# Performance work log

Measured on AMD Instinct MI355X. Metric: run time of the kernel, lower is better.

Reference implementation:

```python
import jax, jax.numpy as jnp
import numpy as np

C = 512

def conv1x1(x, w, b):
    # x: [B,C,H,W], w: [O,C], b: [O]
    return jnp.einsum('bchw,oc->bohw', x, w) + b[None, :, None, None]

def setup_inputs() -> dict:
    key = jax.random.key(0)
    ks = jax.random.split(key, 7)
    s = 1.0 / np.sqrt(C)
    x = jax.random.normal(ks[0], (8, C, 64, 64), dtype=jnp.float32)
    wq = jax.random.uniform(ks[1], (C, C), jnp.float32, -s, s)
    bq = jax.random.uniform(ks[2], (C,), jnp.float32, -s, s)
    wk = jax.random.uniform(ks[3], (C, C), jnp.float32, -s, s)
    bk = jax.random.uniform(ks[4], (C,), jnp.float32, -s, s)
    wv = jax.random.uniform(ks[5], (C, C), jnp.float32, -s, s)
    bv = jax.random.uniform(ks[6], (C,), jnp.float32, -s, s)
    return {"x": x, "wq": wq, "bq": bq, "wk": wk, "bk": bk, "wv": wv, "bv": bv}

def reference(x, wq, bq, wk, bk, wv, bv):
    B, Cc, H, W = x.shape
    q = conv1x1(x, wq, bq).reshape(B, Cc, H * W)   # [B,C,N]
    k = conv1x1(x, wk, bk).reshape(B, Cc, H * W)   # [B,C,N]
    v = conv1x1(x, wv, bv).reshape(B, Cc, H * W)   # [B,C,N]
    attn = jnp.einsum('bcn,bdn->bcd', q, k)        # q @ k^T over spatial dim -> [B,C,C]
    attn = jax.nn.softmax(attn, axis=-1)
    out = jnp.einsum('bcd,bdn->bcn', attn, v).reshape(B, Cc, H, W)
    return out + x
```

## Files before the change

kernel.cpp:

```cpp
#include <hip/hip_runtime.h>
#include <cstdint>

typedef unsigned short u16;
typedef unsigned int   u32;
typedef _Float16 f16;

typedef __attribute__((ext_vector_type(8))) _Float16 f16x8;
typedef __attribute__((ext_vector_type(4))) float    f32x4;

__device__ __forceinline__ u16 f2h(float f) {
    union { f16 h; u16 u; } c; c.h = (f16)f; return c.u;
}
__device__ __forceinline__ float h2f(u16 u) {
    union { u16 u; f16 h; } c; c.u = u; return (float)c.h;
}

__device__ __forceinline__ void async_copy16(const u16* g, u16* lds) {
    __builtin_amdgcn_global_load_lds(
        (const __attribute__((address_space(1))) void*)g,
        (__attribute__((address_space(3))) void*)lds,
        16, 0, 0);
}

__device__ __forceinline__ void gemm_nt_f16(
    u16* smem, const u16* __restrict__ A, int lda,
    const u16* __restrict__ B, int ldb, int K, f32x4 acc[4][4])
{
    u16* As = smem; u16* Bs = smem + 4096;
    const int t = threadIdx.x, w = t >> 6, lane = t & 63;
    const int srow = lane >> 2;
    const int skc  = (((lane & 3) ^ ((lane >> 3) & 3)) * 8);
    const int ra0 = (w*2+0)*16 + srow, ra1 = (w*2+1)*16 + srow;
    const u16* gA0 = A + (size_t)ra0 * lda + skc;
    const u16* gA1 = A + (size_t)ra1 * lda + skc;
    const u16* gB0 = B + (size_t)ra0 * ldb + skc;
    const u16* gB1 = B + (size_t)ra1 * ldb + skc;
    u16* lA0 = As + (w*2+0)*512; u16* lA1 = As + (w*2+1)*512;
    u16* lB0 = Bs + (w*2+0)*512; u16* lB1 = Bs + (w*2+1)*512;
    const int fr = lane & 15, fq = lane >> 4;
    const int fc = (fq ^ ((fr >> 1) & 3)) * 8;
    const int wm = (w >> 1) * 64, wn = (w & 1) * 64;
    const u16* fA = As + (wm + fr) * 32 + fc;
    const u16* fB = Bs + (wn + fr) * 32 + fc;

    for (int k0 = 0; k0 < K; k0 += 32) {
        async_copy16(gA0 + k0, lA0);
        async_copy16(gA1 + k0, lA1);
        async_copy16(gB0 + k0, lB0);
        async_copy16(gB1 + k0, lB1);
        __syncthreads();
        f16x8 af[4], bf[4];
#pragma unroll
        for (int i = 0; i < 4; i++) af[i] = *(const f16x8*)(fA + i * 512);
#pragma unroll
        for (int i = 0; i < 4; i++) bf[i] = *(const f16x8*)(fB + i * 512);
#pragma unroll
        for (int mi = 0; mi < 4; mi++)
#pragma unroll
            for (int ni = 0; ni < 4; ni++)
                acc[mi][ni] = __builtin_amdgcn_mfma_f32_16x16x32_f16(
                    af[mi], bf[ni], acc[mi][ni], 0, 0, 0);
        __syncthreads();
    }
}

__device__ __forceinline__ void zero_acc(f32x4 acc[4][4]) {
#pragma unroll
    for (int i = 0; i < 4; i++)
#pragma unroll
        for (int j = 0; j < 4; j++) {
            f32x4 z = {0.f, 0.f, 0.f, 0.f};
            acc[i][j] = z;
        }
}

__global__ __launch_bounds__(256) void k_convw(const float* __restrict__ wq,
                                               const float* __restrict__ wk,
                                               const float* __restrict__ wv,
                                               u16* __restrict__ Wf)
{
    const int t = blockIdx.x * 256 + threadIdx.x;
    const int e = t * 4;
    const int sel = e >> 18;
    const int off = e & 262143;
    const float* src = (sel == 0) ? wq : (sel == 1) ? wk : wv;
    float4 v = *(const float4*)(src + off);
    ushort4 h;
    h.x = f2h(v.x); h.y = f2h(v.y); h.z = f2h(v.z); h.w = f2h(v.w);
    *(ushort4*)(Wf + sel * 262144 + off) = h;
}

__global__ __launch_bounds__(256) void k_transpose(const float* __restrict__ x,
                                                   u16* __restrict__ XT)
{
    __shared__ u16 tile[64][70];
    const int t  = threadIdx.x;
    const int b  = blockIdx.z;
    const int c0 = blockIdx.y * 64;
    const int n0 = blockIdx.x * 64;
    const int rr   = t >> 4;
    const int col4 = (t & 15) * 4;

    const float* src = x + ((size_t)b * 512 + c0) * 4096 + n0;
#pragma unroll
    for (int i = 0; i < 4; i++) {
        int row = i * 16 + rr;
        float4 v = *(const float4*)(src + (size_t)row * 4096 + col4);
        ushort4 h;
        h.x = f2h(v.x); h.y = f2h(v.y); h.z = f2h(v.z); h.w = f2h(v.w);
        *(ushort4*)&tile[row][col4] = h;
    }
    __syncthreads();
    u16* dst = XT + ((size_t)b * 4096 + n0) * 512 + c0;
#pragma unroll
    for (int i = 0; i < 4; i++) {
        int nrow = i * 16 + rr;
        ushort4 o;
        o.x = tile[col4 + 0][nrow];
        o.y = tile[col4 + 1][nrow];
        o.z = tile[col4 + 2][nrow];
        o.w = tile[col4 + 3][nrow];
        *(ushort4*)(dst + (size_t)nrow * 512 + col4) = o;
    }
}

__global__ __launch_bounds__(256) void k_qkv(
    const u16* __restrict__ Wf,
    const float* __restrict__ bq, const float* __restrict__ bk, const float* __restrict__ bv,
    const u16* __restrict__ XT,
    u16* __restrict__ Qh, u16* __restrict__ Kh, u16* __restrict__ VT)
{
    __shared__ u16 smem[8192];
    const int n0  = blockIdx.x * 128;
    const int my  = blockIdx.y;
    const int b   = blockIdx.z;
    const int sel = my >> 2;
    const int m0  = (my & 3) * 128;

    const float* bi = (sel == 0) ? bq : (sel == 1) ? bk : bv;
    const u16* Ap = Wf + (size_t)sel * 262144 + (size_t)m0 * 512;
    const u16* Bp = XT + ((size_t)b * 4096 + n0) * 512;

    f32x4 acc[4][4];
    zero_acc(acc);
    gemm_nt_f16(smem, Ap, 512, Bp, 512, 512, acc);

    const int t = threadIdx.x, w = t >> 6, lane = t & 63;
    const int wm = (w >> 1) * 64, wn = (w & 1) * 64;
    const int cn = lane & 15, cq = lane >> 4;

    if (sel < 2) {
        u16* out = ((sel == 0) ? Qh : Kh) + (size_t)b * 512 * 4096;
#pragma unroll
        for (int mi = 0; mi < 4; mi++)
#pragma unroll
            for (int ni = 0; ni < 4; ni++)
#pragma unroll
                for (int r = 0; r < 4; r++) {
                    int m = wm + mi * 16 + cq * 4 + r;
                    int n = wn + ni * 16 + cn;
                    out[(size_t)(m0 + m) * 4096 + n0 + n] =
                        f2h(acc[mi][ni][r] + bi[m0 + m]);
                }
    } else {
        u16* out = VT + (size_t)b * 4096 * 512;
#pragma unroll
        for (int mi = 0; mi < 4; mi++)
#pragma unroll
            for (int ni = 0; ni < 4; ni++) {
                int n  = wn + ni * 16 + cn;
                int mb = wm + mi * 16 + cq * 4;
                ushort4 pk;
                pk.x = f2h(acc[mi][ni][0] + bi[m0 + mb + 0]);
                pk.y = f2h(acc[mi][ni][1] + bi[m0 + mb + 1]);
                pk.z = f2h(acc[mi][ni][2] + bi[m0 + mb + 2]);
                pk.w = f2h(acc[mi][ni][3] + bi[m0 + mb + 3]);
                *(ushort4*)(out + (size_t)(n0 + n) * 512 + m0 + mb) = pk;
            }
    }
}

__global__ __launch_bounds__(256) void k_scores(const u16* __restrict__ Qh,
                                                const u16* __restrict__ Kh,
                                                float* __restrict__ S)
{
    __shared__ u16 smem[8192];
    const int n0 = blockIdx.x * 128;
    const int m0 = blockIdx.y * 128;
    const int bz = blockIdx.z;
    const int b  = bz >> 2, ks = bz & 3;

    const u16* Ap = Qh + (size_t)b * 512 * 4096 + (size_t)m0 * 4096 + ks * 1024;
    const u16* Bp = Kh + (size_t)b * 512 * 4096 + (size_t)n0 * 4096 + ks * 1024;

    f32x4 acc[4][4];
    zero_acc(acc);
    gemm_nt_f16(smem, Ap, 4096, Bp, 4096, 1024, acc);

    const int t = threadIdx.x, w = t >> 6, lane = t & 63;
    const int wm = (w >> 1) * 64, wn = (w & 1) * 64;
    const int cn = lane & 15, cq = lane >> 4;

    float* out = S + ((size_t)(ks * 8 + b) * 512 + m0) * 512 + n0;
#pragma unroll
    for (int mi = 0; mi < 4; mi++)
#pragma unroll
        for (int ni = 0; ni < 4; ni++)
#pragma unroll
            for (int r = 0; r < 4; r++) {
                int m = wm + mi * 16 + cq * 4 + r;
                int n = wn + ni * 16 + cn;
                out[(size_t)m * 512 + n] = acc[mi][ni][r];
            }
}

__global__ __launch_bounds__(256) void k_softmax(const float* __restrict__ S,
                                                 u16* __restrict__ P)
{
    const int row = blockIdx.x;
    const int t = threadIdx.x, w = t >> 6, lane = t & 63;
    const size_t st = (size_t)8 * 512 * 512;
    const float* r0 = S + (size_t)row * 512;

    float v0 = r0[t]       + r0[t + st]       + r0[t + 2*st]       + r0[t + 3*st];
    float v1 = r0[t + 256] + r0[t + 256 + st] + r0[t + 256 + 2*st] + r0[t + 256 + 3*st];

    float m = fmaxf(v0, v1);
    for (int o = 32; o; o >>= 1) m = fmaxf(m, __shfl_xor(m, o));
    __shared__ float redm[4];
    if (lane == 0) redm[w] = m;
    __syncthreads();
    m = fmaxf(fmaxf(redm[0], redm[1]), fmaxf(redm[2], redm[3]));

    float e0 = __expf(v0 - m), e1 = __expf(v1 - m);
    float s = e0 + e1;
    for (int o = 32; o; o >>= 1) s += __shfl_xor(s, o);
    __shared__ float reds[4];
    if (lane == 0) reds[w] = s;
    __syncthreads();
    s = reds[0] + reds[1] + reds[2] + reds[3];

    float inv = 1.0f / s;
    P[(size_t)row * 512 + t]       = f2h(e0 * inv);
    P[(size_t)row * 512 + t + 256] = f2h(e1 * inv);
}

__global__ __launch_bounds__(256) void k_out(const u16* __restrict__ P,
                                             const u16* __restrict__ VT,
                                             const float* __restrict__ x,
                                             float* __restrict__ out)
{
    __shared__ u16 smem[8192];
    const int n0 = blockIdx.x * 128;
    const int m0 = blockIdx.y * 128;
    const int b  = blockIdx.z;

    const u16* Ap = P  + (size_t)b * 512 * 512 + (size_t)m0 * 512;
    const u16* Bp = VT + (size_t)b * 4096 * 512 + (size_t)n0 * 512;

    f32x4 acc[4][4];
    zero_acc(acc);
    gemm_nt_f16(smem, Ap, 512, Bp, 512, 512, acc);

    const int t = threadIdx.x, w = t >> 6, lane = t & 63;
    const int wm = (w >> 1) * 64, wn = (w & 1) * 64;
    const int cn = lane & 15, cq = lane >> 4;

#pragma unroll
    for (int mi = 0; mi < 4; mi++)
#pragma unroll
        for (int ni = 0; ni < 4; ni++)
#pragma unroll
            for (int r = 0; r < 4; r++) {
                int m = wm + mi * 16 + cq * 4 + r;
                int n = wn + ni * 16 + cn;
                size_t idx = ((size_t)b * 512 + m0 + m) * 4096 + n0 + n;
                out[idx] = acc[mi][ni][r] + x[idx];
            }
}

extern "C" void kernel_launch(void* const* d_in, const int* in_sizes, int n_in,
                              void* d_out, int out_size, void* d_ws, size_t ws_size,
                              hipStream_t stream)
{
    const float* x  = (const float*)d_in[0];
    const float* wq = (const float*)d_in[1];
    const float* bq = (const float*)d_in[2];
    const float* wk = (const float*)d_in[3];
    const float* bk = (const float*)d_in[4];
    const float* wv = (const float*)d_in[5];
    const float* bv = (const float*)d_in[6];
    float* out = (float*)d_out;

    char* ws = (char*)d_ws;
    u16*  Wf = (u16*)(ws);
    u16*  XT = (u16*)(ws + 1572864);
    u16*  Qh = (u16*)(ws + 35127296);
    u16*  Kh = (u16*)(ws + 68681728);
    u16*  VT = (u16*)(ws + 102236160);
    float* S = (float*)(ws + 1572864);
    u16*  P  = (u16*)(ws + 135790592);

    k_convw<<<dim3(768), dim3(256), 0, stream>>>(wq, wk, wv, Wf);
    k_transpose<<<dim3(64, 8, 8), dim3(256), 0, stream>>>(x, XT);
    k_qkv<<<dim3(32, 12, 8), dim3(256), 0, stream>>>(Wf, bq, bk, bv, XT, Qh, Kh, VT);
    k_scores<<<dim3(4, 4, 32), dim3(256), 0, stream>>>(Qh, Kh, S);
    k_softmax<<<dim3(4096), dim3(256), 0, stream>>>(S, P);
    k_out<<<dim3(32, 4, 8), dim3(256), 0, stream>>>(P, VT, x, out);
}
```

Before: 295.2 us.

## Fuse x transpose and fp16 conversion into QKV GEMM B-tile loading

Removes the separate transpose kernel and the XT workspace. The QKV GEMM now reads fp32 x directly, converts it to fp16 in registers and writes it transposed into a swizzled LDS tile. The next k-slice is prefetched into registers while the current MFMAs run. This avoids writing and re-reading a 32MB intermediate and one launch. The cost is that x is re-read as fp32 by 12 blocks per tile (across m and q/k/v) with strided scalar loads instead of async LDS copies.

```diff
diff --git a/kernel.cpp b/kernel.cpp
--- a/kernel.cpp
+++ b/kernel.cpp
@@ -10,9 +10,6 @@
 
 __device__ __forceinline__ u16 f2h(float f) {
     union { f16 h; u16 u; } c; c.h = (f16)f; return c.u;
-}
-__device__ __forceinline__ float h2f(u16 u) {
-    union { u16 u; f16 h; } c; c.u = u; return (float)c.h;
 }
 
 __device__ __forceinline__ void async_copy16(const u16* g, u16* lds) {
@@ -90,47 +87,14 @@
     *(ushort4*)(Wf + sel * 262144 + off) = h;
 }
 
-__global__ __launch_bounds__(256) void k_transpose(const float* __restrict__ x,
-                                                   u16* __restrict__ XT)
-{
-    __shared__ u16 tile[64][70];
-    const int t  = threadIdx.x;
-    const int b  = blockIdx.z;
-    const int c0 = blockIdx.y * 64;
-    const int n0 = blockIdx.x * 64;
-    const int rr   = t >> 4;
-    const int col4 = (t & 15) * 4;
-
-    const float* src = x + ((size_t)b * 512 + c0) * 4096 + n0;
-#pragma unroll
-    for (int i = 0; i < 4; i++) {
-        int row = i * 16 + rr;
-        float4 v = *(const float4*)(src + (size_t)row * 4096 + col4);
-        ushort4 h;
-        h.x = f2h(v.x); h.y = f2h(v.y); h.z = f2h(v.z); h.w = f2h(v.w);
-        *(ushort4*)&tile[row][col4] = h;
-    }
-    __syncthreads();
-    u16* dst = XT + ((size_t)b * 4096 + n0) * 512 + c0;
-#pragma unroll
-    for (int i = 0; i < 4; i++) {
-        int nrow = i * 16 + rr;
-        ushort4 o;
-        o.x = tile[col4 + 0][nrow];
-        o.y = tile[col4 + 1][nrow];
-        o.z = tile[col4 + 2][nrow];
-        o.w = tile[col4 + 3][nrow];
-        *(ushort4*)(dst + (size_t)nrow * 512 + col4) = o;
-    }
-}
-
 __global__ __launch_bounds__(256) void k_qkv(
     const u16* __restrict__ Wf,
     const float* __restrict__ bq, const float* __restrict__ bk, const float* __restrict__ bv,
-    const u16* __restrict__ XT,
+    const float* __restrict__ x,
     u16* __restrict__ Qh, u16* __restrict__ Kh, u16* __restrict__ VT)
 {
     __shared__ u16 smem[8192];
+    u16* As = smem; u16* Bs = smem + 4096;
     const int n0  = blockIdx.x * 128;
     const int my  = blockIdx.y;
     const int b   = blockIdx.z;
@@ -138,15 +102,71 @@
     const int m0  = (my & 3) * 128;
 
     const float* bi = (sel == 0) ? bq : (sel == 1) ? bk : bv;
-    const u16* Ap = Wf + (size_t)sel * 262144 + (size_t)m0 * 512;
-    const u16* Bp = XT + ((size_t)b * 4096 + n0) * 512;
+    const u16* A = Wf + (size_t)sel * 262144 + (size_t)m0 * 512;
+
+    const int t = threadIdx.x, w = t >> 6, lane = t & 63;
+
+    const int srow = lane >> 2;
+    const int skc  = (((lane & 3) ^ ((lane >> 3) & 3)) * 8);
+    const int ra0 = (w*2+0)*16 + srow, ra1 = (w*2+1)*16 + srow;
+    const u16* gA0 = A + (size_t)ra0 * 512 + skc;
+    const u16* gA1 = A + (size_t)ra1 * 512 + skc;
+    u16* lA0 = As + (w*2+0)*512; u16* lA1 = As + (w*2+1)*512;
+
+    const int nn = t & 15;
+    const int cg = t >> 4;
+    const float* xb = x + ((size_t)b * 512 + 2 * cg) * 4096 + n0 + nn;
+    const int chunkB = (cg >> 2) ^ ((nn >> 1) & 3);
+    u16* lB = Bs + nn * 32 + chunkB * 8 + ((2 * cg) & 7);
+
+    const int fr = lane & 15, fq = lane >> 4;
+    const int fc = (fq ^ ((fr >> 1) & 3)) * 8;
+    const int wm = (w >> 1) * 64, wn = (w & 1) * 64;
+    const u16* fA = As + (wm + fr) * 32 + fc;
+    const u16* fB = Bs + (wn + fr) * 32 + fc;
 
     f32x4 acc[4][4];
     zero_acc(acc);
-    gemm_nt_f16(smem, Ap, 512, Bp, 512, 512, acc);
-
-    const int t = threadIdx.x, w = t >> 6, lane = t & 63;
-    const int wm = (w >> 1) * 64, wn = (w & 1) * 64;
+
+    float va[8], vb[8];
+#pragma unroll
+    for (int nb = 0; nb < 8; nb++) {
+        va[nb] = xb[nb * 16];
+        vb[nb] = xb[4096 + nb * 16];
+    }
+
+    for (int k0 = 0; k0 < 512; k0 += 32) {
+        async_copy16(gA0 + k0, lA0);
+        async_copy16(gA1 + k0, lA1);
+#pragma unroll
+        for (int nb = 0; nb < 8; nb++) {
+            u32 pk = (u32)f2h(va[nb]) | ((u32)f2h(vb[nb]) << 16);
+            *(u32*)(lB + nb * 512) = pk;
+        }
+        __syncthreads();
+
+        const int kn = (k0 + 32 < 512) ? (k0 + 32) : 0;
+        const float* xk = xb + (size_t)kn * 4096;
+#pragma unroll
+        for (int nb = 0; nb < 8; nb++) {
+            va[nb] = xk[nb * 16];
+            vb[nb] = xk[4096 + nb * 16];
+        }
+
+        f16x8 af[4], bf[4];
+#pragma unroll
+        for (int i = 0; i < 4; i++) af[i] = *(const f16x8*)(fA + i * 512);
+#pragma unroll
+        for (int i = 0; i < 4; i++) bf[i] = *(const f16x8*)(fB + i * 512);
+#pragma unroll
+        for (int mi = 0; mi < 4; mi++)
+#pragma unroll
+            for (int ni = 0; ni < 4; ni++)
+                acc[mi][ni] = __builtin_amdgcn_mfma_f32_16x16x32_f16(
+                    af[mi], bf[ni], acc[mi][ni], 0, 0, 0);
+        __syncthreads();
+    }
+
     const int cn = lane & 15, cq = lane >> 4;
 
     if (sel < 2) {
@@ -294,16 +314,14 @@
 
     char* ws = (char*)d_ws;
     u16*  Wf = (u16*)(ws);
-    u16*  XT = (u16*)(ws + 1572864);
-    u16*  Qh = (u16*)(ws + 35127296);
-    u16*  Kh = (u16*)(ws + 68681728);
-    u16*  VT = (u16*)(ws + 102236160);
-    float* S = (float*)(ws + 1572864);
+    u16*  Qh = (u16*)(ws + 1572864);
+    u16*  Kh = (u16*)(ws + 35127296);
+    u16*  VT = (u16*)(ws + 68681728);
+    float* S = (float*)(ws + 102236160);
     u16*  P  = (u16*)(ws + 135790592);
 
     k_convw<<<dim3(768), dim3(256), 0, stream>>>(wq, wk, wv, Wf);
-    k_transpose<<<dim3(64, 8, 8), dim3(256), 0, stream>>>(x, XT);
-    k_qkv<<<dim3(32, 12, 8), dim3(256), 0, stream>>>(Wf, bq, bk, bv, XT, Qh, Kh, VT);
+    k_qkv<<<dim3(32, 12, 8), dim3(256), 0, stream>>>(Wf, bq, bk, bv, x, Qh, Kh, VT);
     k_scores<<<dim3(4, 4, 32), dim3(256), 0, stream>>>(Qh, Kh, S);
     k_softmax<<<dim3(4096), dim3(256), 0, stream>>>(S, P);
     k_out<<<dim3(32, 4, 8), dim3(256), 0, stream>>>(P, VT, x, out);
```

New measurement: 331.6 us. +12.3%, slower.

## Compute Q and K projections together in one block sharing the X tile

Applied to the files above, without the earlier changes.

The QKV projection kernel now gives the Q and K projections for the same output rows to a single block. That block loads the transposed-input tile once and issues MFMAs into two accumulator sets, while V keeps the original path. This cuts the global and LDS traffic for the shared B operand and reduces the grid from 12 to 8 y-blocks. In exchange, the Q/K blocks hold twice the accumulator registers and more LDS, which may reduce occupancy, and they are heavier than the V blocks, which unbalances the grid.

```diff
diff --git a/kernel.cpp b/kernel.cpp
--- a/kernel.cpp
+++ b/kernel.cpp
@@ -10,9 +10,6 @@
 
 __device__ __forceinline__ u16 f2h(float f) {
     union { f16 h; u16 u; } c; c.h = (f16)f; return c.u;
-}
-__device__ __forceinline__ float h2f(u16 u) {
-    union { u16 u; f16 h; } c; c.u = u; return (float)c.h;
 }
 
 __device__ __forceinline__ void async_copy16(const u16* g, u16* lds) {
@@ -130,27 +127,71 @@
     const u16* __restrict__ XT,
     u16* __restrict__ Qh, u16* __restrict__ Kh, u16* __restrict__ VT)
 {
-    __shared__ u16 smem[8192];
-    const int n0  = blockIdx.x * 128;
-    const int my  = blockIdx.y;
-    const int b   = blockIdx.z;
-    const int sel = my >> 2;
-    const int m0  = (my & 3) * 128;
-
-    const float* bi = (sel == 0) ? bq : (sel == 1) ? bk : bv;
-    const u16* Ap = Wf + (size_t)sel * 262144 + (size_t)m0 * 512;
-    const u16* Bp = XT + ((size_t)b * 4096 + n0) * 512;
-
-    f32x4 acc[4][4];
-    zero_acc(acc);
-    gemm_nt_f16(smem, Ap, 512, Bp, 512, 512, acc);
-
-    const int t = threadIdx.x, w = t >> 6, lane = t & 63;
+    __shared__ u16 smem[12288];
+    const int n0 = blockIdx.x * 128;
+    const int my = blockIdx.y;
+    const int b  = blockIdx.z;
+    const int t = threadIdx.x, w = t >> 6, lane = t & 63;
+    const int srow = lane >> 2;
+    const int skc  = (((lane & 3) ^ ((lane >> 3) & 3)) * 8);
+    const int ra0 = (w*2+0)*16 + srow, ra1 = (w*2+1)*16 + srow;
+    const int fr = lane & 15, fq = lane >> 4;
+    const int fc = (fq ^ ((fr >> 1) & 3)) * 8;
     const int wm = (w >> 1) * 64, wn = (w & 1) * 64;
     const int cn = lane & 15, cq = lane >> 4;
 
-    if (sel < 2) {
-        u16* out = ((sel == 0) ? Qh : Kh) + (size_t)b * 512 * 4096;
+    const u16* Bp  = XT + ((size_t)b * 4096 + n0) * 512;
+    const u16* gB0 = Bp + (size_t)ra0 * 512 + skc;
+    const u16* gB1 = Bp + (size_t)ra1 * 512 + skc;
+
+    if (my < 4) {
+        const int m0 = my * 128;
+        u16* Asq = smem; u16* Ask = smem + 4096; u16* Bs = smem + 8192;
+        const u16* Aq = Wf + (size_t)m0 * 512;
+        const u16* Ak = Wf + 262144 + (size_t)m0 * 512;
+        const u16* gq0 = Aq + (size_t)ra0 * 512 + skc;
+        const u16* gq1 = Aq + (size_t)ra1 * 512 + skc;
+        const u16* gk0 = Ak + (size_t)ra0 * 512 + skc;
+        const u16* gk1 = Ak + (size_t)ra1 * 512 + skc;
+        u16* lq0 = Asq + (w*2+0)*512; u16* lq1 = Asq + (w*2+1)*512;
+        u16* lk0 = Ask + (w*2+0)*512; u16* lk1 = Ask + (w*2+1)*512;
+        u16* lB0 = Bs  + (w*2+0)*512; u16* lB1 = Bs  + (w*2+1)*512;
+        const u16* fAq = Asq + (wm + fr) * 32 + fc;
+        const u16* fAk = Ask + (wm + fr) * 32 + fc;
+        const u16* fB  = Bs  + (wn + fr) * 32 + fc;
+
+        f32x4 accq[4][4], acck[4][4];
+        zero_acc(accq); zero_acc(acck);
+
+        for (int k0 = 0; k0 < 512; k0 += 32) {
+            async_copy16(gq0 + k0, lq0);
+            async_copy16(gq1 + k0, lq1);
+            async_copy16(gk0 + k0, lk0);
+            async_copy16(gk1 + k0, lk1);
+            async_copy16(gB0 + k0, lB0);
+            async_copy16(gB1 + k0, lB1);
+            __syncthreads();
+            f16x8 aq[4], ak[4], bf[4];
+#pragma unroll
+            for (int i = 0; i < 4; i++) {
+                aq[i] = *(const f16x8*)(fAq + i * 512);
+                ak[i] = *(const f16x8*)(fAk + i * 512);
+                bf[i] = *(const f16x8*)(fB  + i * 512);
+            }
+#pragma unroll
+            for (int mi = 0; mi < 4; mi++)
+#pragma unroll
+                for (int ni = 0; ni < 4; ni++) {
+                    accq[mi][ni] = __builtin_amdgcn_mfma_f32_16x16x32_f16(
+                        aq[mi], bf[ni], accq[mi][ni], 0, 0, 0);
+                    acck[mi][ni] = __builtin_amdgcn_mfma_f32_16x16x32_f16(
+                        ak[mi], bf[ni], acck[mi][ni], 0, 0, 0);
+                }
+            __syncthreads();
+        }
+
+        u16* oq = Qh + (size_t)b * 512 * 4096;
+        u16* ok = Kh + (size_t)b * 512 * 4096;
 #pragma unroll
         for (int mi = 0; mi < 4; mi++)
 #pragma unroll
@@ -159,10 +200,18 @@
                 for (int r = 0; r < 4; r++) {
                     int m = wm + mi * 16 + cq * 4 + r;
                     int n = wn + ni * 16 + cn;
-                    out[(size_t)(m0 + m) * 4096 + n0 + n] =
-                        f2h(acc[mi][ni][r] + bi[m0 + m]);
+                    size_t idx = (size_t)(m0 + m) * 4096 + n0 + n;
+                    oq[idx] = f2h(accq[mi][ni][r] + bq[m0 + m]);
+                    ok[idx] = f2h(acck[mi][ni][r] + bk[m0 + m]);
                 }
     } else {
+        const int m0 = (my - 4) * 128;
+        const u16* Ap = Wf + (size_t)2 * 262144 + (size_t)m0 * 512;
+
+        f32x4 acc[4][4];
+        zero_acc(acc);
+        gemm_nt_f16(smem, Ap, 512, Bp, 512, 512, acc);
+
         u16* out = VT + (size_t)b * 4096 * 512;
 #pragma unroll
         for (int mi = 0; mi < 4; mi++)
@@ -171,10 +220,10 @@
                 int n  = wn + ni * 16 + cn;
                 int mb = wm + mi * 16 + cq * 4;
                 ushort4 pk;
-                pk.x = f2h(acc[mi][ni][0] + bi[m0 + mb + 0]);
-                pk.y = f2h(acc[mi][ni][1] + bi[m0 + mb + 1]);
-                pk.z = f2h(acc[mi][ni][2] + bi[m0 + mb + 2]);
-                pk.w = f2h(acc[mi][ni][3] + bi[m0 + mb + 3]);
+                pk.x = f2h(acc[mi][ni][0] + bv[m0 + mb + 0]);
+                pk.y = f2h(acc[mi][ni][1] + bv[m0 + mb + 1]);
+                pk.z = f2h(acc[mi][ni][2] + bv[m0 + mb + 2]);
+                pk.w = f2h(acc[mi][ni][3] + bv[m0 + mb + 3]);
                 *(ushort4*)(out + (size_t)(n0 + n) * 512 + m0 + mb) = pk;
             }
     }
@@ -303,7 +352,7 @@
 
     k_convw<<<dim3(768), dim3(256), 0, stream>>>(wq, wk, wv, Wf);
     k_transpose<<<dim3(64, 8, 8), dim3(256), 0, stream>>>(x, XT);
-    k_qkv<<<dim3(32, 12, 8), dim3(256), 0, stream>>>(Wf, bq, bk, bv, XT, Qh, Kh, VT);
+    k_qkv<<<dim3(32, 8, 8), dim3(256), 0, stream>>>(Wf, bq, bk, bv, XT, Qh, Kh, VT);
     k_scores<<<dim3(4, 4, 32), dim3(256), 0, stream>>>(Qh, Kh, S);
     k_softmax<<<dim3(4096), dim3(256), 0, stream>>>(S, P);
     k_out<<<dim3(32, 4, 8), dim3(256), 0, stream>>>(P, VT, x, out);
```

New measurement: 315.1 us. +6.7%, slower.
